# Optimization experiments

Hardware: AMD Instinct MI355X
Metric: run time of the kernel (lower is better)

Reference implementation:

```python
import jax, jax.numpy as jnp
import numpy as np

IN_DIM = 512
INTER_DIM = 512
OUT_DIM = 512
NUM_GROUPS = 16
N = 8192
EPS = 1e-5


def setup_inputs() -> dict:
    key = jax.random.key(0)
    ks = jax.random.split(key, 14)
    s_in = 1.0 / np.sqrt(IN_DIM)
    s_inter = 1.0 / np.sqrt(INTER_DIM)
    s_hid = 1.0 / np.sqrt(OUT_DIM)
    return {
        "x": jax.random.normal(ks[0], (N, IN_DIM), dtype=jnp.float32),
        "D": jax.random.uniform(ks[1], (N, N), dtype=jnp.float32),
        "Wq": jax.random.uniform(ks[2], (IN_DIM, INTER_DIM), minval=-s_in, maxval=s_in),
        "bq": jax.random.uniform(ks[3], (INTER_DIM,), minval=-s_in, maxval=s_in),
        "Wk": jax.random.uniform(ks[4], (IN_DIM, INTER_DIM), minval=-s_in, maxval=s_in),
        "bk": jax.random.uniform(ks[5], (INTER_DIM,), minval=-s_in, maxval=s_in),
        "Wv": jax.random.uniform(ks[6], (IN_DIM, INTER_DIM), minval=-s_in, maxval=s_in),
        "bv": jax.random.uniform(ks[7], (INTER_DIM,), minval=-s_in, maxval=s_in),
        "Wf": jax.random.uniform(ks[8], (INTER_DIM, OUT_DIM), minval=-s_inter, maxval=s_inter),
        "bf": jax.random.uniform(ks[9], (OUT_DIM,), minval=-s_inter, maxval=s_inter),
        "Wp": jax.random.uniform(ks[10], (OUT_DIM, OUT_DIM), minval=-s_hid, maxval=s_hid),
        "bp": jax.random.uniform(ks[11], (OUT_DIM,), minval=-s_hid, maxval=s_hid),
        "gamma": jnp.ones((OUT_DIM,), dtype=jnp.float32),
        "beta": jnp.zeros((OUT_DIM,), dtype=jnp.float32),
    }


def group_norm(x, gamma, beta):
    # x: (N, C); normalize each sample over groups of C//G channels
    n, c = x.shape
    xg = x.reshape(n, NUM_GROUPS, c // NUM_GROUPS)
    mu = jnp.mean(xg, axis=-1, keepdims=True)
    var = jnp.var(xg, axis=-1, keepdims=True)
    xn = ((xg - mu) * jax.lax.rsqrt(var + EPS)).reshape(n, c)
    return xn * gamma + beta


def reference(x, D, Wq, bq, Wk, bk, Wv, bv, Wf, bf, Wp, bp, gamma, beta):
    Q = x @ Wq + bq                      # (N, inter)
    K = x @ Wk + bk                      # (N, inter)
    V = x @ Wv + bv                      # (N, inter)
    inter_feat = Q @ K.T                 # (N, N) -- full retention matrix
    x_ret = (D * inter_feat) @ V         # (N, inter)
    h = jax.nn.gelu(x_ret @ Wf + bf, approximate=False)  # (N, out)
    out = h @ Wp + bp                    # (N, out)
    return group_norm(out, gamma, beta)
```

## Files before the change

### kernel.cpp

```cpp
#include <hip/hip_runtime.h>
#include <hip/hip_fp16.h>
#include <math.h>

#define NROWS 8192
#define DIM 512

typedef _Float16 half8 __attribute__((ext_vector_type(8)));
typedef _Float16 half4 __attribute__((ext_vector_type(4)));
typedef float f32x4 __attribute__((ext_vector_type(4)));

__device__ __forceinline__ f32x4 mfma16(half8 a, half8 b, f32x4 c) {
  return __builtin_amdgcn_mfma_f32_16x16x32_f16(a, b, c, 0, 0, 0);
}

__global__ __launch_bounds__(256) void prep(
    const float* __restrict__ x,
    const float* __restrict__ Wq, const float* __restrict__ Wk,
    const float* __restrict__ Wv, const float* __restrict__ Wf,
    const float* __restrict__ Wp,
    _Float16* __restrict__ xh, _Float16* __restrict__ WT)
{
  const int bid = blockIdx.x, tid = threadIdx.x;
  if (bid < 256) {
    const int base = bid * 16384 + tid * 4;
    #pragma unroll
    for (int r = 0; r < 16; ++r) {
      float4 v = *(const float4*)(x + base + r * 1024);
      half4 h;
      h[0] = (_Float16)v.x; h[1] = (_Float16)v.y;
      h[2] = (_Float16)v.z; h[3] = (_Float16)v.w;
      *(half4*)(xh + base + r * 1024) = h;
    }
  } else {
    const int wb = bid - 256;
    const int wi = wb >> 7;
    const int th = (wb & 127) * 256 + tid;
    const int n = th >> 6, kc = th & 63;
    const float* W = (wi == 0) ? Wq : (wi == 1) ? Wk : (wi == 2) ? Wv
                   : (wi == 3) ? Wf : Wp;
    half8 h;
    #pragma unroll
    for (int j = 0; j < 8; ++j) h[j] = (_Float16)W[(size_t)(kc * 8 + j) * 512 + n];
    *(half8*)(WT + (size_t)wi * 262144 + (size_t)n * 512 + kc * 8) = h;
  }
}

__global__ __launch_bounds__(512, 2) void qkv(
    const _Float16* __restrict__ xh, const _Float16* __restrict__ WT,
    const float* __restrict__ bq, const float* __restrict__ bk,
    const float* __restrict__ bv,
    _Float16* __restrict__ Qh, _Float16* __restrict__ Kh,
    _Float16* __restrict__ Vt)
{
  __shared__ _Float16 As[32][520];
  const int M0 = blockIdx.x * 32;
  const int tid = threadIdx.x;
  const int lane = tid & 63;
  const int w = tid >> 6;
  const int lr = lane & 15;
  const int lkb = lane >> 4;

  #pragma unroll
  for (int j = 0; j < 4; ++j) {
    int c = tid + 512 * j;
    int r = c >> 6, c16 = c & 63;
    half8 h = *(const half8*)(xh + (size_t)(M0 + r) * 512 + c16 * 8);
    *(half8*)&As[r][c16 * 8] = h;
  }
  __syncthreads();

  const _Float16* WqT = WT;
  const _Float16* WkT = WT + 262144;
  const _Float16* WvT = WT + 524288;

  f32x4 aq[2][4] = {}, ak[2][4] = {}, av[2][4] = {};

  for (int ks = 0; ks < 16; ++ks) {
    half8 a0 = *(const half8*)&As[lr][ks * 32 + lkb * 8];
    half8 a1 = *(const half8*)&As[16 + lr][ks * 32 + lkb * 8];
    #pragma unroll
    for (int nt = 0; nt < 4; ++nt) {
      const size_t boff = (size_t)(w * 64 + nt * 16 + lr) * 512 + ks * 32 + lkb * 8;
      half8 bqf = *(const half8*)(WqT + boff);
      half8 bkf = *(const half8*)(WkT + boff);
      half8 bvf = *(const half8*)(WvT + boff);
      aq[0][nt] = mfma16(a0, bqf, aq[0][nt]);
      aq[1][nt] = mfma16(a1, bqf, aq[1][nt]);
      ak[0][nt] = mfma16(a0, bkf, ak[0][nt]);
      ak[1][nt] = mfma16(a1, bkf, ak[1][nt]);
      av[0][nt] = mfma16(a0, bvf, av[0][nt]);
      av[1][nt] = mfma16(a1, bvf, av[1][nt]);
    }
  }

  #pragma unroll
  for (int mt = 0; mt < 2; ++mt) {
    #pragma unroll
    for (int nt = 0; nt < 4; ++nt) {
      const int col = w * 64 + nt * 16 + lr;
      const float vbq = bq[col], vbk = bk[col], vbv = bv[col];
      const int row0 = M0 + mt * 16 + lkb * 4;
      #pragma unroll
      for (int i = 0; i < 4; ++i) {
        Qh[(size_t)(row0 + i) * 512 + col] = (_Float16)(aq[mt][nt][i] + vbq);
        Kh[(size_t)(row0 + i) * 512 + col] = (_Float16)(ak[mt][nt][i] + vbk);
      }
      half4 pk;
      #pragma unroll
      for (int i = 0; i < 4; ++i) pk[i] = (_Float16)(av[mt][nt][i] + vbv);
      *(half4*)(Vt + (size_t)col * NROWS + row0) = pk;
    }
  }
}

__global__ __launch_bounds__(512, 2) void retention(
    const _Float16* __restrict__ Qh, const _Float16* __restrict__ Kh,
    const _Float16* __restrict__ Vt, const float* __restrict__ D,
    float* __restrict__ Xp0, float* __restrict__ Xp1)
{
  __shared__ _Float16 Ks[2][32][520];
  __shared__ _Float16 Vs[2][512][40];
  __shared__ _Float16 Ps[64][40];

  const int bid = blockIdx.x;
  const int Jc = bid & 1;
  const int I0 = (bid >> 1) * 64;
  const int Jbase = Jc * 4096;
  float* __restrict__ Xp = Jc ? Xp1 : Xp0;

  const int tid = threadIdx.x;
  const int lane = tid & 63;
  const int w = tid >> 6;
  const int wr = w >> 1;
  const int wc = w & 1;
  const int lr = lane & 15;
  const int lkb = lane >> 4;

  half8 q[16];
  {
    const _Float16* qrow = Qh + (size_t)(I0 + wr * 16 + lr) * 512 + lkb * 8;
    #pragma unroll
    for (int ks = 0; ks < 16; ++ks) q[ks] = *(const half8*)(qrow + ks * 32);
  }

  int kr[4], kc16[4], vn[4], vjc[4];
  #pragma unroll
  for (int j = 0; j < 4; ++j) {
    int c = tid + 512 * j;
    kr[j] = c >> 6;  kc16[j] = c & 63;
    vn[j] = c >> 2;  vjc[j]  = c & 3;
  }

  {
    #pragma unroll
    for (int j = 0; j < 4; ++j) {
      half8 kd = *(const half8*)(Kh + (size_t)(Jbase + kr[j]) * 512 + kc16[j] * 8);
      half8 vd = *(const half8*)(Vt + (size_t)vn[j] * NROWS + Jbase + vjc[j] * 8);
      *(half8*)&Ks[0][kr[j]][kc16[j] * 8] = kd;
      *(half8*)&Vs[0][vn[j]][vjc[j] * 8] = vd;
    }
  }
  __syncthreads();

  f32x4 acc[16] = {};

  for (int t = 0; t < 128; ++t) {
    const int cur = t & 1;
    const int Jb = Jbase + t * 32;
    const bool more = (t + 1 < 128);

    half8 kd[4], vd[4];
    if (more) {
      const int Jn = Jb + 32;
      #pragma unroll
      for (int j = 0; j < 4; ++j) {
        kd[j] = *(const half8*)(Kh + (size_t)(Jn + kr[j]) * 512 + kc16[j] * 8);
        vd[j] = *(const half8*)(Vt + (size_t)vn[j] * NROWS + Jn + vjc[j] * 8);
      }
    }

    float dv[4];
    #pragma unroll
    for (int i = 0; i < 4; ++i)
      dv[i] = D[(size_t)(I0 + wr * 16 + lkb * 4 + i) * NROWS + Jb + wc * 16 + lr];

    f32x4 s[4] = {};
    #pragma unroll
    for (int ks = 0; ks < 16; ++ks) {
      half8 kb = *(const half8*)&Ks[cur][wc * 16 + lr][ks * 32 + lkb * 8];
      s[ks & 3] = mfma16(q[ks], kb, s[ks & 3]);
    }
    #pragma unroll
    for (int i = 0; i < 4; ++i) {
      float sv = (s[0][i] + s[1][i]) + (s[2][i] + s[3][i]);
      Ps[wr * 16 + lkb * 4 + i][wc * 16 + lr] = (_Float16)(sv * dv[i]);
    }
    __syncthreads();

    half8 pa = *(const half8*)&Ps[wr * 16 + lr][lkb * 8];
    #pragma unroll
    for (int nt = 0; nt < 16; ++nt) {
      half8 vb = *(const half8*)&Vs[cur][wc * 256 + nt * 16 + lr][lkb * 8];
      acc[nt] = mfma16(pa, vb, acc[nt]);
    }

    if (more) {
      #pragma unroll
      for (int j = 0; j < 4; ++j) {
        *(half8*)&Ks[cur ^ 1][kr[j]][kc16[j] * 8] = kd[j];
        *(half8*)&Vs[cur ^ 1][vn[j]][vjc[j] * 8] = vd[j];
      }
    }
    __syncthreads();
  }

  #pragma unroll
  for (int nt = 0; nt < 16; ++nt) {
    #pragma unroll
    for (int i = 0; i < 4; ++i)
      Xp[(size_t)(I0 + wr * 16 + lkb * 4 + i) * 512 + wc * 256 + nt * 16 + lr] =
          acc[nt][i];
  }
}

__global__ __launch_bounds__(512, 2) void mlp1(
    const float* __restrict__ Xp0, const float* __restrict__ Xp1,
    const _Float16* __restrict__ WfT, const float* __restrict__ bf,
    _Float16* __restrict__ Hh)
{
  __shared__ _Float16 As[32][520];
  const int M0 = blockIdx.x * 32;
  const int tid = threadIdx.x;
  const int lane = tid & 63;
  const int w = tid >> 6;
  const int lr = lane & 15;
  const int lkb = lane >> 4;

  #pragma unroll
  for (int j = 0; j < 4; ++j) {
    int c = tid + 512 * j;
    int r = c >> 6, c16 = c & 63;
    const size_t off = (size_t)(M0 + r) * 512 + c16 * 8;
    float4 a0 = *(const float4*)(Xp0 + off);
    float4 a1 = *(const float4*)(Xp0 + off + 4);
    float4 b0 = *(const float4*)(Xp1 + off);
    float4 b1 = *(const float4*)(Xp1 + off + 4);
    half8 h;
    h[0] = (_Float16)(a0.x + b0.x); h[1] = (_Float16)(a0.y + b0.y);
    h[2] = (_Float16)(a0.z + b0.z); h[3] = (_Float16)(a0.w + b0.w);
    h[4] = (_Float16)(a1.x + b1.x); h[5] = (_Float16)(a1.y + b1.y);
    h[6] = (_Float16)(a1.z + b1.z); h[7] = (_Float16)(a1.w + b1.w);
    *(half8*)&As[r][c16 * 8] = h;
  }
  __syncthreads();

  f32x4 acc[2][4] = {};
  for (int ks = 0; ks < 16; ++ks) {
    half8 a0 = *(const half8*)&As[lr][ks * 32 + lkb * 8];
    half8 a1 = *(const half8*)&As[16 + lr][ks * 32 + lkb * 8];
    #pragma unroll
    for (int nt = 0; nt < 4; ++nt) {
      half8 bfr = *(const half8*)(WfT + (size_t)(w * 64 + nt * 16 + lr) * 512 +
                                  ks * 32 + lkb * 8);
      acc[0][nt] = mfma16(a0, bfr, acc[0][nt]);
      acc[1][nt] = mfma16(a1, bfr, acc[1][nt]);
    }
  }

  #pragma unroll
  for (int mt = 0; mt < 2; ++mt) {
    #pragma unroll
    for (int nt = 0; nt < 4; ++nt) {
      const int col = w * 64 + nt * 16 + lr;
      const float bias = bf[col];
      #pragma unroll
      for (int i = 0; i < 4; ++i) {
        float v = acc[mt][nt][i] + bias;
        v = 0.5f * v * (1.0f + erff(v * 0.70710678118f));
        Hh[(size_t)(M0 + mt * 16 + lkb * 4 + i) * 512 + col] = (_Float16)v;
      }
    }
  }
}

__global__ __launch_bounds__(512, 2) void mlp2(
    const _Float16* __restrict__ Hh, const _Float16* __restrict__ WpT,
    const float* __restrict__ bp, const float* __restrict__ gamma,
    const float* __restrict__ beta, float* __restrict__ out)
{
  __shared__ _Float16 As[32][520];
  const int M0 = blockIdx.x * 32;
  const int tid = threadIdx.x;
  const int lane = tid & 63;
  const int w = tid >> 6;
  const int lr = lane & 15;
  const int lkb = lane >> 4;

  #pragma unroll
  for (int j = 0; j < 4; ++j) {
    int c = tid + 512 * j;
    int r = c >> 6, c16 = c & 63;
    half8 h = *(const half8*)(Hh + (size_t)(M0 + r) * 512 + c16 * 8);
    *(half8*)&As[r][c16 * 8] = h;
  }
  __syncthreads();

  f32x4 acc[2][4] = {};
  for (int ks = 0; ks < 16; ++ks) {
    half8 a0 = *(const half8*)&As[lr][ks * 32 + lkb * 8];
    half8 a1 = *(const half8*)&As[16 + lr][ks * 32 + lkb * 8];
    #pragma unroll
    for (int nt = 0; nt < 4; ++nt) {
      half8 b = *(const half8*)(WpT + (size_t)(w * 64 + nt * 16 + lr) * 512 +
                                ks * 32 + lkb * 8);
      acc[0][nt] = mfma16(a0, b, acc[0][nt]);
      acc[1][nt] = mfma16(a1, b, acc[1][nt]);
    }
  }

  #pragma unroll
  for (int mt = 0; mt < 2; ++mt) {
    float vv[4][4];
    #pragma unroll
    for (int nt = 0; nt < 4; ++nt) {
      const float bias = bp[w * 64 + nt * 16 + lr];
      #pragma unroll
      for (int i = 0; i < 4; ++i) vv[nt][i] = acc[mt][nt][i] + bias;
    }
    #pragma unroll
    for (int i = 0; i < 4; ++i) {
      float s0 = vv[0][i] + vv[1][i];
      float q0 = vv[0][i] * vv[0][i] + vv[1][i] * vv[1][i];
      float s1 = vv[2][i] + vv[3][i];
      float q1 = vv[2][i] * vv[2][i] + vv[3][i] * vv[3][i];
      #pragma unroll
      for (int m = 1; m <= 8; m <<= 1) {
        s0 += __shfl_xor(s0, m); q0 += __shfl_xor(q0, m);
        s1 += __shfl_xor(s1, m); q1 += __shfl_xor(q1, m);
      }
      const float mu0 = s0 * (1.0f / 32.0f);
      const float rs0 = rsqrtf(q0 * (1.0f / 32.0f) - mu0 * mu0 + 1e-5f);
      const float mu1 = s1 * (1.0f / 32.0f);
      const float rs1 = rsqrtf(q1 * (1.0f / 32.0f) - mu1 * mu1 + 1e-5f);
      const int row = M0 + mt * 16 + lkb * 4 + i;
      #pragma unroll
      for (int nt = 0; nt < 4; ++nt) {
        const int col = w * 64 + nt * 16 + lr;
        const float mu = (nt < 2) ? mu0 : mu1;
        const float rs = (nt < 2) ? rs0 : rs1;
        out[(size_t)row * 512 + col] =
            (vv[nt][i] - mu) * rs * gamma[col] + beta[col];
      }
    }
  }
}

extern "C" void kernel_launch(void* const* d_in, const int* in_sizes, int n_in,
                              void* d_out, int out_size, void* d_ws, size_t ws_size,
                              hipStream_t stream)
{
  const float* x  = (const float*)d_in[0];
  const float* D  = (const float*)d_in[1];
  const float* Wq = (const float*)d_in[2];
  const float* bq = (const float*)d_in[3];
  const float* Wk = (const float*)d_in[4];
  const float* bk = (const float*)d_in[5];
  const float* Wv = (const float*)d_in[6];
  const float* bv = (const float*)d_in[7];
  const float* Wf = (const float*)d_in[8];
  const float* bf = (const float*)d_in[9];
  const float* Wp = (const float*)d_in[10];
  const float* bp = (const float*)d_in[11];
  const float* gamma = (const float*)d_in[12];
  const float* beta  = (const float*)d_in[13];

  char* ws = (char*)d_ws;
  const size_t MB = 1024 * 1024;
  _Float16* xh  = (_Float16*)(ws);
  _Float16* WT  = (_Float16*)(ws + 8 * MB);
  _Float16* Qh  = (_Float16*)(ws + 11 * MB);
  _Float16* Kh  = (_Float16*)(ws + 19 * MB);
  _Float16* Vt  = (_Float16*)(ws + 27 * MB);
  float*    Xp0 = (float*)   (ws + 35 * MB);
  float*    Xp1 = (float*)   (ws + 51 * MB);
  _Float16* Hh  = (_Float16*)(ws);

  hipLaunchKernelGGL(prep, dim3(896), dim3(256), 0, stream,
                     x, Wq, Wk, Wv, Wf, Wp, xh, WT);
  hipLaunchKernelGGL(qkv, dim3(256), dim3(512), 0, stream,
                     xh, WT, bq, bk, bv, Qh, Kh, Vt);
  hipLaunchKernelGGL(retention, dim3(256), dim3(512), 0, stream,
                     Qh, Kh, Vt, D, Xp0, Xp1);
  hipLaunchKernelGGL(mlp1, dim3(256), dim3(512), 0, stream,
                     Xp0, Xp1, WT + 3 * 262144, bf, Hh);
  hipLaunchKernelGGL(mlp2, dim3(256), dim3(512), 0, stream,
                     Hh, WT + 4 * 262144, bp, gamma, beta, (float*)d_out);
}
```

Before: 740.3 us.

## Restructure retention with 64-row K tiles, LDS DMA, swizzling; fuse MLP kernels

The retention kernel now processes 64 key rows per step. K tiles are fetched with global_load_lds DMA into XOR-swizzled shared memory, V fragments are read directly from global memory into registers, and D values are prefetched one step ahead. Explicit waitcnt, barriers, setprio and sched_barrier fences control the overlap. The two MLP kernels are fused so the GELU output stays in LDS, and the weight transpose in prep goes through shared memory for coalesced reads. The hand scheduling is brittle, and the direct V global loads could add latency.

```diff
diff --git a/kernel.cpp b/kernel.cpp
--- a/kernel.cpp
+++ b/kernel.cpp
@@ -3,7 +3,6 @@
 #include <math.h>
 
 #define NROWS 8192
-#define DIM 512
 
 typedef _Float16 half8 __attribute__((ext_vector_type(8)));
 typedef _Float16 half4 __attribute__((ext_vector_type(4)));
@@ -11,6 +10,14 @@
 
 __device__ __forceinline__ f32x4 mfma16(half8 a, half8 b, f32x4 c) {
   return __builtin_amdgcn_mfma_f32_16x16x32_f16(a, b, c, 0, 0, 0);
+}
+
+#define SFENCE __builtin_amdgcn_sched_barrier(0)
+
+__device__ __forceinline__ void dma16(const _Float16* g, _Float16* l) {
+  __builtin_amdgcn_global_load_lds(
+      (const __attribute__((address_space(1))) void*)g,
+      (__attribute__((address_space(3))) void*)l, 16, 0, 0);
 }
 
 __global__ __launch_bounds__(256) void prep(
@@ -20,10 +27,11 @@
     const float* __restrict__ Wp,
     _Float16* __restrict__ xh, _Float16* __restrict__ WT)
 {
+  __shared__ float Ws[64][68];
   const int bid = blockIdx.x, tid = threadIdx.x;
   if (bid < 256) {
     const int base = bid * 16384 + tid * 4;
-    #pragma unroll
+#pragma unroll
     for (int r = 0; r < 16; ++r) {
       float4 v = *(const float4*)(x + base + r * 1024);
       half4 h;
@@ -33,15 +41,28 @@
     }
   } else {
     const int wb = bid - 256;
-    const int wi = wb >> 7;
-    const int th = (wb & 127) * 256 + tid;
-    const int n = th >> 6, kc = th & 63;
+    const int wi = wb >> 6;
+    const int tix = wb & 63;
+    const int k0 = (tix >> 3) * 64;
+    const int n0 = (tix & 7) * 64;
     const float* W = (wi == 0) ? Wq : (wi == 1) ? Wk : (wi == 2) ? Wv
                    : (wi == 3) ? Wf : Wp;
-    half8 h;
-    #pragma unroll
-    for (int j = 0; j < 8; ++j) h[j] = (_Float16)W[(size_t)(kc * 8 + j) * 512 + n];
-    *(half8*)(WT + (size_t)wi * 262144 + (size_t)n * 512 + kc * 8) = h;
+    const int r = tid >> 2, cq = tid & 3;
+#pragma unroll
+    for (int j = 0; j < 4; ++j) {
+      float4 v = *(const float4*)(W + (size_t)(k0 + r) * 512 + n0 + cq * 16 + j * 4);
+      *(float4*)&Ws[r][cq * 16 + j * 4] = v;
+    }
+    __syncthreads();
+    const int n = tid >> 2, kq = tid & 3;
+    half8 h0, h1;
+#pragma unroll
+    for (int m = 0; m < 8; ++m) h0[m] = (_Float16)Ws[kq * 16 + m][n];
+#pragma unroll
+    for (int m = 0; m < 8; ++m) h1[m] = (_Float16)Ws[kq * 16 + 8 + m][n];
+    _Float16* dst = WT + (size_t)wi * 262144 + (size_t)(n0 + n) * 512 + k0 + kq * 16;
+    *(half8*)dst = h0;
+    *(half8*)(dst + 8) = h1;
   }
 }
 
@@ -60,7 +81,7 @@
   const int lr = lane & 15;
   const int lkb = lane >> 4;
 
-  #pragma unroll
+#pragma unroll
   for (int j = 0; j < 4; ++j) {
     int c = tid + 512 * j;
     int r = c >> 6, c16 = c & 63;
@@ -78,7 +99,7 @@
   for (int ks = 0; ks < 16; ++ks) {
     half8 a0 = *(const half8*)&As[lr][ks * 32 + lkb * 8];
     half8 a1 = *(const half8*)&As[16 + lr][ks * 32 + lkb * 8];
-    #pragma unroll
+#pragma unroll
     for (int nt = 0; nt < 4; ++nt) {
       const size_t boff = (size_t)(w * 64 + nt * 16 + lr) * 512 + ks * 32 + lkb * 8;
       half8 bqf = *(const half8*)(WqT + boff);
@@ -93,20 +114,20 @@
     }
   }
 
-  #pragma unroll
+#pragma unroll
   for (int mt = 0; mt < 2; ++mt) {
-    #pragma unroll
+#pragma unroll
     for (int nt = 0; nt < 4; ++nt) {
       const int col = w * 64 + nt * 16 + lr;
       const float vbq = bq[col], vbk = bk[col], vbv = bv[col];
       const int row0 = M0 + mt * 16 + lkb * 4;
-      #pragma unroll
+#pragma unroll
       for (int i = 0; i < 4; ++i) {
         Qh[(size_t)(row0 + i) * 512 + col] = (_Float16)(aq[mt][nt][i] + vbq);
         Kh[(size_t)(row0 + i) * 512 + col] = (_Float16)(ak[mt][nt][i] + vbk);
       }
       half4 pk;
-      #pragma unroll
+#pragma unroll
       for (int i = 0; i < 4; ++i) pk[i] = (_Float16)(av[mt][nt][i] + vbv);
       *(half4*)(Vt + (size_t)col * NROWS + row0) = pk;
     }
@@ -118,9 +139,8 @@
     const _Float16* __restrict__ Vt, const float* __restrict__ D,
     float* __restrict__ Xp0, float* __restrict__ Xp1)
 {
-  __shared__ _Float16 Ks[2][32][520];
-  __shared__ _Float16 Vs[2][512][40];
-  __shared__ _Float16 Ps[64][40];
+  __shared__ _Float16 Ks[2][64][512];
+  __shared__ _Float16 Ps[2][64][64];
 
   const int bid = blockIdx.x;
   const int Jc = bid & 1;
@@ -131,102 +151,133 @@
   const int tid = threadIdx.x;
   const int lane = tid & 63;
   const int w = tid >> 6;
-  const int wr = w >> 1;
-  const int wc = w & 1;
+  const int wr = w >> 2;
+  const int wc = w & 3;
   const int lr = lane & 15;
   const int lkb = lane >> 4;
 
-  half8 q[16];
-  {
-    const _Float16* qrow = Qh + (size_t)(I0 + wr * 16 + lr) * 512 + lkb * 8;
-    #pragma unroll
-    for (int ks = 0; ks < 16; ++ks) q[ks] = *(const half8*)(qrow + ks * 32);
-  }
-
-  int kr[4], kc16[4], vn[4], vjc[4];
-  #pragma unroll
-  for (int j = 0; j < 4; ++j) {
-    int c = tid + 512 * j;
-    kr[j] = c >> 6;  kc16[j] = c & 63;
-    vn[j] = c >> 2;  vjc[j]  = c & 3;
-  }
-
-  {
-    #pragma unroll
-    for (int j = 0; j < 4; ++j) {
-      half8 kd = *(const half8*)(Kh + (size_t)(Jbase + kr[j]) * 512 + kc16[j] * 8);
-      half8 vd = *(const half8*)(Vt + (size_t)vn[j] * NROWS + Jbase + vjc[j] * 8);
-      *(half8*)&Ks[0][kr[j]][kc16[j] * 8] = kd;
-      *(half8*)&Vs[0][vn[j]][vjc[j] * 8] = vd;
-    }
-  }
-  __syncthreads();
-
-  f32x4 acc[16] = {};
-
-  for (int t = 0; t < 128; ++t) {
-    const int cur = t & 1;
-    const int Jb = Jbase + t * 32;
-    const bool more = (t + 1 < 128);
-
-    half8 kd[4], vd[4];
-    if (more) {
-      const int Jn = Jb + 32;
-      #pragma unroll
-      for (int j = 0; j < 4; ++j) {
-        kd[j] = *(const half8*)(Kh + (size_t)(Jn + kr[j]) * 512 + kc16[j] * 8);
-        vd[j] = *(const half8*)(Vt + (size_t)vn[j] * NROWS + Jn + vjc[j] * 8);
-      }
-    }
-
-    float dv[4];
-    #pragma unroll
+  half8 q[2][16];
+#pragma unroll
+  for (int it = 0; it < 2; ++it) {
+    const _Float16* qp = Qh + (size_t)(I0 + wr * 32 + it * 16 + lr) * 512 + lkb * 8;
+#pragma unroll
+    for (int kc = 0; kc < 16; ++kc) q[it][kc] = *(const half8*)(qp + kc * 32);
+  }
+
+#pragma unroll
+  for (int rr = 0; rr < 8; ++rr) {
+    const int row = w * 8 + rr;
+    dma16(Kh + (size_t)(Jbase + row) * 512 + ((lane ^ (row & 7)) * 8), &Ks[0][row][0]);
+  }
+  SFENCE;
+  float dv[8];
+#pragma unroll
+  for (int it = 0; it < 2; ++it)
+#pragma unroll
     for (int i = 0; i < 4; ++i)
-      dv[i] = D[(size_t)(I0 + wr * 16 + lkb * 4 + i) * NROWS + Jb + wc * 16 + lr];
-
-    f32x4 s[4] = {};
-    #pragma unroll
-    for (int ks = 0; ks < 16; ++ks) {
-      half8 kb = *(const half8*)&Ks[cur][wc * 16 + lr][ks * 32 + lkb * 8];
-      s[ks & 3] = mfma16(q[ks], kb, s[ks & 3]);
-    }
-    #pragma unroll
-    for (int i = 0; i < 4; ++i) {
-      float sv = (s[0][i] + s[1][i]) + (s[2][i] + s[3][i]);
-      Ps[wr * 16 + lkb * 4 + i][wc * 16 + lr] = (_Float16)(sv * dv[i]);
-    }
-    __syncthreads();
-
-    half8 pa = *(const half8*)&Ps[wr * 16 + lr][lkb * 8];
-    #pragma unroll
-    for (int nt = 0; nt < 16; ++nt) {
-      half8 vb = *(const half8*)&Vs[cur][wc * 256 + nt * 16 + lr][lkb * 8];
-      acc[nt] = mfma16(pa, vb, acc[nt]);
-    }
-
-    if (more) {
-      #pragma unroll
-      for (int j = 0; j < 4; ++j) {
-        *(half8*)&Ks[cur ^ 1][kr[j]][kc16[j] * 8] = kd[j];
-        *(half8*)&Vs[cur ^ 1][vn[j]][vjc[j] * 8] = vd[j];
-      }
-    }
-    __syncthreads();
-  }
-
-  #pragma unroll
-  for (int nt = 0; nt < 16; ++nt) {
-    #pragma unroll
-    for (int i = 0; i < 4; ++i)
-      Xp[(size_t)(I0 + wr * 16 + lkb * 4 + i) * 512 + wc * 256 + nt * 16 + lr] =
-          acc[nt][i];
-  }
-}
-
-__global__ __launch_bounds__(512, 2) void mlp1(
+      dv[it * 4 + i] = D[(size_t)(I0 + wr * 32 + it * 16 + lkb * 4 + i) * NROWS +
+                         Jbase + wc * 16 + lr];
+  asm volatile("s_waitcnt vmcnt(0)" ::: "memory");
+  SFENCE;
+  __builtin_amdgcn_s_barrier();
+
+  f32x4 acc[4][4] = {};
+  const int jrow = wc * 16 + lr;
+
+  for (int t = 0; t < 64; ++t) {
+    const int cb = t & 1;
+    const int tn = (t + 1 < 64) ? t + 1 : 63;
+    const int J0 = Jbase + t * 64;
+    const int J0n = Jbase + tn * 64;
+
+    half8 vreg[4][2];
+#pragma unroll
+    for (int nt = 0; nt < 4; ++nt)
+#pragma unroll
+      for (int k2 = 0; k2 < 2; ++k2)
+        vreg[nt][k2] = *(const half8*)(Vt + (size_t)(w * 64 + nt * 16 + lr) * NROWS +
+                                       J0 + k2 * 32 + lkb * 8);
+    SFENCE;
+
+    f32x4 s0 = {}, s1 = {};
+    const _Float16* ksb = &Ks[cb][0][0];
+    __builtin_amdgcn_s_setprio(1);
+#pragma unroll
+    for (int kc = 0; kc < 16; ++kc) {
+      half8 kb = *(const half8*)(ksb + jrow * 512 + (((kc * 4 + lkb) ^ (jrow & 7)) * 8));
+      s0 = mfma16(q[0][kc], kb, s0);
+      s1 = mfma16(q[1][kc], kb, s1);
+    }
+    __builtin_amdgcn_s_setprio(0);
+    SFENCE;
+
+#pragma unroll
+    for (int rr = 0; rr < 8; ++rr) {
+      const int row = w * 8 + rr;
+      dma16(Kh + (size_t)(J0n + row) * 512 + ((lane ^ (row & 7)) * 8),
+            &Ks[cb ^ 1][row][0]);
+    }
+    SFENCE;
+
+    _Float16* psb = &Ps[cb][0][0];
+#pragma unroll
+    for (int it = 0; it < 2; ++it)
+#pragma unroll
+      for (int i = 0; i < 4; ++i) {
+        const int prow = wr * 32 + it * 16 + lkb * 4 + i;
+        const float sv = (it == 0 ? s0[i] : s1[i]) * dv[it * 4 + i];
+        psb[prow * 64 + (((wc * 2 + (lr >> 3)) ^ (prow & 7)) * 8) + (lr & 7)] =
+            (_Float16)sv;
+      }
+
+#pragma unroll
+    for (int it = 0; it < 2; ++it)
+#pragma unroll
+      for (int i = 0; i < 4; ++i)
+        dv[it * 4 + i] = D[(size_t)(I0 + wr * 32 + it * 16 + lkb * 4 + i) * NROWS +
+                           J0n + wc * 16 + lr];
+    SFENCE;
+
+    asm volatile("s_waitcnt lgkmcnt(0)" ::: "memory");
+    SFENCE;
+    __builtin_amdgcn_s_barrier();
+
+    __builtin_amdgcn_s_setprio(1);
+#pragma unroll
+    for (int k2 = 0; k2 < 2; ++k2)
+#pragma unroll
+      for (int it = 0; it < 4; ++it) {
+        const int prow = it * 16 + lr;
+        half8 pa = *(const half8*)(psb + prow * 64 +
+                                   (((k2 * 4 + lkb) ^ (prow & 7)) * 8));
+#pragma unroll
+        for (int nt = 0; nt < 4; ++nt)
+          acc[it][nt] = mfma16(pa, vreg[nt][k2], acc[it][nt]);
+      }
+    __builtin_amdgcn_s_setprio(0);
+    SFENCE;
+
+    asm volatile("s_waitcnt vmcnt(0)" ::: "memory");
+    SFENCE;
+    __builtin_amdgcn_s_barrier();
+  }
+
+#pragma unroll
+  for (int it = 0; it < 4; ++it)
+#pragma unroll
+    for (int nt = 0; nt < 4; ++nt)
+#pragma unroll
+      for (int i = 0; i < 4; ++i)
+        Xp[(size_t)(I0 + it * 16 + lkb * 4 + i) * 512 + w * 64 + nt * 16 + lr] =
+            acc[it][nt][i];
+}
+
+__global__ __launch_bounds__(512, 2) void mlp(
     const float* __restrict__ Xp0, const float* __restrict__ Xp1,
     const _Float16* __restrict__ WfT, const float* __restrict__ bf,
-    _Float16* __restrict__ Hh)
+    const _Float16* __restrict__ WpT, const float* __restrict__ bp,
+    const float* __restrict__ gamma, const float* __restrict__ beta,
+    float* __restrict__ out)
 {
   __shared__ _Float16 As[32][520];
   const int M0 = blockIdx.x * 32;
@@ -236,7 +287,7 @@
   const int lr = lane & 15;
   const int lkb = lane >> 4;
 
-  #pragma unroll
+#pragma unroll
   for (int j = 0; j < 4; ++j) {
     int c = tid + 512 * j;
     int r = c >> 6, c16 = c & 63;
@@ -258,82 +309,60 @@
   for (int ks = 0; ks < 16; ++ks) {
     half8 a0 = *(const half8*)&As[lr][ks * 32 + lkb * 8];
     half8 a1 = *(const half8*)&As[16 + lr][ks * 32 + lkb * 8];
-    #pragma unroll
-    for (int nt = 0; nt < 4; ++nt) {
-      half8 bfr = *(const half8*)(WfT + (size_t)(w * 64 + nt * 16 + lr) * 512 +
-                                  ks * 32 + lkb * 8);
-      acc[0][nt] = mfma16(a0, bfr, acc[0][nt]);
-      acc[1][nt] = mfma16(a1, bfr, acc[1][nt]);
-    }
-  }
-
-  #pragma unroll
-  for (int mt = 0; mt < 2; ++mt) {
-    #pragma unroll
+#pragma unroll
+    for (int nt = 0; nt < 4; ++nt) {
+      half8 b = *(const half8*)(WfT + (size_t)(w * 64 + nt * 16 + lr) * 512 +
+                                ks * 32 + lkb * 8);
+      acc[0][nt] = mfma16(a0, b, acc[0][nt]);
+      acc[1][nt] = mfma16(a1, b, acc[1][nt]);
+    }
+  }
+  __syncthreads();
+
+#pragma unroll
+  for (int mt = 0; mt < 2; ++mt)
+#pragma unroll
     for (int nt = 0; nt < 4; ++nt) {
       const int col = w * 64 + nt * 16 + lr;
       const float bias = bf[col];
-      #pragma unroll
+#pragma unroll
       for (int i = 0; i < 4; ++i) {
         float v = acc[mt][nt][i] + bias;
         v = 0.5f * v * (1.0f + erff(v * 0.70710678118f));
-        Hh[(size_t)(M0 + mt * 16 + lkb * 4 + i) * 512 + col] = (_Float16)v;
-      }
-    }
-  }
-}
-
-__global__ __launch_bounds__(512, 2) void mlp2(
-    const _Float16* __restrict__ Hh, const _Float16* __restrict__ WpT,
-    const float* __restrict__ bp, const float* __restrict__ gamma,
-    const float* __restrict__ beta, float* __restrict__ out)
-{
-  __shared__ _Float16 As[32][520];
-  const int M0 = blockIdx.x * 32;
-  const int tid = threadIdx.x;
-  const int lane = tid & 63;
-  const int w = tid >> 6;
-  const int lr = lane & 15;
-  const int lkb = lane >> 4;
-
-  #pragma unroll
-  for (int j = 0; j < 4; ++j) {
-    int c = tid + 512 * j;
-    int r = c >> 6, c16 = c & 63;
-    half8 h = *(const half8*)(Hh + (size_t)(M0 + r) * 512 + c16 * 8);
-    *(half8*)&As[r][c16 * 8] = h;
-  }
+        As[mt * 16 + lkb * 4 + i][col] = (_Float16)v;
+      }
+    }
   __syncthreads();
 
-  f32x4 acc[2][4] = {};
+  f32x4 acc2[2][4] = {};
   for (int ks = 0; ks < 16; ++ks) {
     half8 a0 = *(const half8*)&As[lr][ks * 32 + lkb * 8];
     half8 a1 = *(const half8*)&As[16 + lr][ks * 32 + lkb * 8];
-    #pragma unroll
+#pragma unroll
     for (int nt = 0; nt < 4; ++nt) {
       half8 b = *(const half8*)(WpT + (size_t)(w * 64 + nt * 16 + lr) * 512 +
                                 ks * 32 + lkb * 8);
-      acc[0][nt] = mfma16(a0, b, acc[0][nt]);
-      acc[1][nt] = mfma16(a1, b, acc[1][nt]);
-    }
-  }
-
-  #pragma unroll
+      acc2[0][nt] = mfma16(a0, b, acc2[0][nt]);
+      acc2[1][nt] = mfma16(a1, b, acc2[1][nt]);
+    }
+  }
+
+#pragma unroll
   for (int mt = 0; mt < 2; ++mt) {
     float vv[4][4];
-    #pragma unroll
+#pragma unroll
     for (int nt = 0; nt < 4; ++nt) {
       const float bias = bp[w * 64 + nt * 16 + lr];
-      #pragma unroll
-      for (int i = 0; i < 4; ++i) vv[nt][i] = acc[mt][nt][i] + bias;
-    }
-    #pragma unroll
+#pragma unroll
+      for (int i = 0; i < 4; ++i) vv[nt][i] = acc2[mt][nt][i] + bias;
+    }
+#pragma unroll
     for (int i = 0; i < 4; ++i) {
       float s0 = vv[0][i] + vv[1][i];
       float q0 = vv[0][i] * vv[0][i] + vv[1][i] * vv[1][i];
       float s1 = vv[2][i] + vv[3][i];
       float q1 = vv[2][i] * vv[2][i] + vv[3][i] * vv[3][i];
-      #pragma unroll
+#pragma unroll
       for (int m = 1; m <= 8; m <<= 1) {
         s0 += __shfl_xor(s0, m); q0 += __shfl_xor(q0, m);
         s1 += __shfl_xor(s1, m); q1 += __shfl_xor(q1, m);
@@ -343,7 +372,7 @@
       const float mu1 = s1 * (1.0f / 32.0f);
       const float rs1 = rsqrtf(q1 * (1.0f / 32.0f) - mu1 * mu1 + 1e-5f);
       const int row = M0 + mt * 16 + lkb * 4 + i;
-      #pragma unroll
+#pragma unroll
       for (int nt = 0; nt < 4; ++nt) {
         const int col = w * 64 + nt * 16 + lr;
         const float mu = (nt < 2) ? mu0 : mu1;
@@ -383,16 +412,14 @@
   _Float16* Vt  = (_Float16*)(ws + 27 * MB);
   float*    Xp0 = (float*)   (ws + 35 * MB);
   float*    Xp1 = (float*)   (ws + 51 * MB);
-  _Float16* Hh  = (_Float16*)(ws);
-
-  hipLaunchKernelGGL(prep, dim3(896), dim3(256), 0, stream,
+
+  hipLaunchKernelGGL(prep, dim3(576), dim3(256), 0, stream,
                      x, Wq, Wk, Wv, Wf, Wp, xh, WT);
   hipLaunchKernelGGL(qkv, dim3(256), dim3(512), 0, stream,
                      xh, WT, bq, bk, bv, Qh, Kh, Vt);
   hipLaunchKernelGGL(retention, dim3(256), dim3(512), 0, stream,
                      Qh, Kh, Vt, D, Xp0, Xp1);
-  hipLaunchKernelGGL(mlp1, dim3(256), dim3(512), 0, stream,
-                     Xp0, Xp1, WT + 3 * 262144, bf, Hh);
-  hipLaunchKernelGGL(mlp2, dim3(256), dim3(512), 0, stream,
-                     Hh, WT + 4 * 262144, bp, gamma, beta, (float*)d_out);
-}
+  hipLaunchKernelGGL(mlp, dim3(256), dim3(512), 0, stream,
+                     Xp0, Xp1, WT + 3 * 262144, bf, WT + 4 * 262144, bp,
+                     gamma, beta, (float*)d_out);
+}
```

New measurement: 1.222 ms. +65.1%, slower.
